# Kernel tuning notes

Measured on AMD Instinct MI355X. Metric: run time of the kernel, lower is better.

Reference implementation:

```python
import jax, jax.numpy as jnp
import numpy as np

B, N, T = 2, 512, 4096
D_MODEL, N_MODES, NODE_H, EDGE_H = 128, 32, 128, 256


def _lin(key, d_in, d_out, scale=0.02):
    kw, kb = jax.random.split(key)
    W = jax.random.normal(kw, (d_in, d_out), jnp.float32) * scale
    b = jax.random.normal(kb, (d_out,), jnp.float32) * scale
    return W, b


def setup_inputs() -> dict:
    key = jax.random.key(0)
    ks = jax.random.split(key, 12)
    spikes = jax.random.normal(ks[0], (B, N, T), jnp.float32)
    # temporal FNO spectral weights (init * 0.01 as in torch)
    Wr = jax.random.normal(ks[1], (N_MODES, D_MODEL), jnp.float32) * 0.01
    Wi = jax.random.normal(ks[2], (N_MODES, D_MODEL), jnp.float32) * 0.01
    pw1, pb1 = _lin(ks[3], D_MODEL, D_MODEL)
    pw2, pb2 = _lin(ks[4], D_MODEL, D_MODEL)
    nw1, nb1 = _lin(ks[5], D_MODEL, NODE_H)
    nw2, nb2 = _lin(ks[6], NODE_H, D_MODEL)
    sw, sb = _lin(ks[7], D_MODEL, EDGE_H)
    tw, tb = _lin(ks[8], D_MODEL, EDGE_H)
    ew1, eb1 = _lin(ks[9], 2 * EDGE_H, EDGE_H)
    ew2, eb2 = _lin(ks[10], EDGE_H, EDGE_H // 2)
    ew3, eb3 = _lin(ks[11], EDGE_H // 2, 2)
    alpha = jnp.asarray(1.0, jnp.float32)
    beta = jnp.asarray(0.0, jnp.float32)
    return dict(spikes=spikes, Wr=Wr, Wi=Wi, pw1=pw1, pb1=pb1, pw2=pw2, pb2=pb2,
                nw1=nw1, nb1=nb1, nw2=nw2, nb2=nb2, sw=sw, sb=sb, tw=tw, tb=tb,
                ew1=ew1, eb1=eb1, ew2=ew2, eb2=eb2, ew3=ew3, eb3=eb3,
                alpha=alpha, beta=beta)


def reference(spikes, Wr, Wi, pw1, pb1, pw2, pb2, nw1, nb1, nw2, nb2,
              sw, sb, tw, tb, ew1, eb1, ew2, eb2, ew3, eb3, alpha, beta):
    relu = jax.nn.relu
    # --- TemporalFourierOperator1D ---
    xf = jnp.fft.rfft(spikes, axis=-1)[..., :N_MODES]          # [B,N,K] complex
    xr, xi = xf.real.astype(spikes.dtype), xf.imag.astype(spikes.dtype)
    # broadcast complex multiply: [B,N,K,1] x [K,D] -> [B,N,K,D]
    yr = xr[..., None] * Wr - xi[..., None] * Wi
    yi = xr[..., None] * Wi + xi[..., None] * Wr
    E = jnp.sqrt(yr * yr + yi * yi + 1e-8).mean(axis=2)         # [B,N,D]
    E = relu(E @ pw1 + pb1) @ pw2 + pb2                          # post_mlp
    # --- NodeFeatureNet ---
    H = relu(relu(E @ nw1 + nb1) @ nw2 + nb2)                    # [B,N,D]
    # --- EdgeFourierCoeffNet ---
    hs = H @ sw + sb                                             # [B,N,Eh]
    ht = H @ tw + tb
    # concat([hs,ht]) @ ew1 == hs @ ew1[:Eh] + ht @ ew1[Eh:] (exact same math)
    ps = hs @ ew1[:EDGE_H]                                       # [B,N,Eh]
    pt = ht @ ew1[EDGE_H:]
    h = relu(ps[:, :, None, :] + pt[:, None, :, :] + eb1)        # [B,N,N,Eh]
    h = relu(h @ ew2 + eb2)                                      # [B,N,N,Eh/2]
    rt = h @ ew3 + eb3                                           # [B,N,N,2]
    coeffs = rt[..., 0] + 1j * rt[..., 1]                        # [B,N,N] complex
    # --- AdjacencyLinearDecoder2D ---
    adj_spatial = jnp.fft.ifft2(coeffs, axes=(-2, -1)).real
    adj_logits = alpha * adj_spatial + beta
    adj_prob = jax.nn.sigmoid(adj_logits)
    return adj_logits, adj_prob
```

## Files before the change

### kernel.cpp

```cpp
#include <hip/hip_runtime.h>
#include <hip/hip_bf16.h>
#include <math.h>

typedef __attribute__((ext_vector_type(8))) short short8;
typedef __attribute__((ext_vector_type(8))) _Float16 f16x8;
typedef __attribute__((ext_vector_type(4))) float f32x4;

__device__ __forceinline__ short f2bf(float x) {
    union { float f; unsigned u; } v; v.f = x;
    unsigned r = v.u + 0x7fffu + ((v.u >> 16) & 1u);
    return (short)(r >> 16);
}
__device__ __forceinline__ unsigned cvtpk(float lo, float hi) {
    unsigned r;
    asm("v_cvt_pk_bf16_f32 %0, %1, %2" : "=v"(r) : "v"(lo), "v"(hi));
    return r;
}
__device__ __forceinline__ unsigned pk_addrelu(unsigned a, unsigned b) {
    unsigned r;
    asm("v_pk_add_f16 %0, %1, %2\n\tv_pk_max_f16 %0, %0, 0"
        : "=v"(r) : "v"(a), "v"(b));
    return r;
}
__device__ __forceinline__ float bflo(unsigned u) {
    union { unsigned u; float f; } v; v.u = u << 16; return v.f;
}
__device__ __forceinline__ float bfhi(unsigned u) {
    union { unsigned u; float f; } v; v.u = u & 0xffff0000u; return v.f;
}
union U32x4 { unsigned u[4]; short8 s8; };
union U32x4H { unsigned u[4]; f16x8 h8; };

__global__ __launch_bounds__(256) void setup_kernel(const float* __restrict__ ew2,
                                                    const float* __restrict__ pw1, const float* __restrict__ pw2,
                                                    const float* __restrict__ nw1, const float* __restrict__ nw2,
                                                    const float* __restrict__ sw, const float* __restrict__ tw,
                                                    const float* __restrict__ sb, const float* __restrict__ tb,
                                                    const float* __restrict__ ew1, const float* __restrict__ eb1,
                                                    short* __restrict__ W4P, short* __restrict__ F1P,
                                                    short* __restrict__ F2, _Float16* __restrict__ EW2H,
                                                    short* __restrict__ PWP,
                                                    short* __restrict__ WCP, float* __restrict__ BC) {
    __shared__ float2 tab[4096];
    __shared__ float eL2[256][32];
    int blk = blockIdx.x, tid = threadIdx.x;
    if (blk < 32) {
        for (int i = tid; i < 4096; i += 256) {
            float sn, cs; sincospif((float)i * (1.0f / 2048.0f), &sn, &cs);
            tab[i] = make_float2(cs, sn);
        }
        __syncthreads();
        int base = blk * 8192;
        #pragma unroll 4
        for (int u = 0; u < 32; ++u) {
            int i = base + u * 256 + tid;
            int j = i & 7, lane = (i >> 3) & 63, nf = (i >> 9) & 3, kkg = i >> 11;
            int k = kkg * 32 + (lane >> 4) * 8 + j;
            int n = nf * 16 + (lane & 15);
            float2 cs = tab[(k * (n & 31)) & 4095];
            W4P[i] = f2bf(n < 32 ? cs.x : -cs.y);
        }
    } else if (blk < 160) {
        for (int i = tid; i < 512; i += 256) {
            float sn, cs; sincospif((float)i * (1.0f / 256.0f), &sn, &cs);
            tab[i] = make_float2(cs, sn);
        }
        __syncthreads();
        int base = (blk - 32) * 8192;
        #pragma unroll 4
        for (int u = 0; u < 32; ++u) {
            int ii = base + u * 256 + tid;
            int j = ii & 7, lane = (ii >> 3) & 63, nfg = (ii >> 9) & 63, kk = ii >> 15;
            int k2 = kk * 32 + (lane >> 4) * 8 + j;
            int t = k2 >> 1, c = k2 & 1;
            int n = nfg * 16 + (lane & 15);
            int q = n >> 1, d = n & 1;
            float2 cs = tab[(t * q) & 511];
            F1P[ii] = f2bf((c == d) ? cs.x : (c ? -cs.y : cs.y));
        }
    } else if (blk < 224) {
        for (int i = tid; i < 512; i += 256) {
            float sn, cs; sincospif((float)i * (1.0f / 256.0f), &sn, &cs);
            tab[i] = make_float2(cs, sn);
        }
        __syncthreads();
        int base = (blk - 160) * 8192;
        #pragma unroll 4
        for (int u = 0; u < 32; ++u) {
            int ii = base + u * 256 + tid;
            int p = ii >> 10, k2 = ii & 1023;
            int s = k2 >> 1, dd = k2 & 1;
            float2 cs = tab[(p * s) & 511];
            F2[ii] = f2bf(dd ? -cs.y : cs.x);
        }
    } else if (blk < 236) {
        int base = (blk - 224) * 8192;
        #pragma unroll 4
        for (int u = 0; u < 32; ++u) {
            int ii = base + u * 256 + tid;
            if (ii < 32768) {
                int j = ii & 7, lane = (ii >> 3) & 63, hf = (ii >> 9) & 7, kk = ii >> 12;
                int k = kk * 32 + (lane >> 4) * 8 + j;
                int h = hf * 16 + (lane & 15);
                EW2H[ii] = (_Float16)ew2[k * 128 + h];
            } else {
                int iw = ii - 32768;
                int l = iw >> 14;
                int r = iw & 16383;
                int j = r & 7, lane = (r >> 3) & 63, nf = (r >> 9) & 7, kk = r >> 12;
                int k = kk * 32 + (lane >> 4) * 8 + j;
                int n = nf * 16 + (lane & 15);
                const float* W = (l == 0) ? pw1 : (l == 1) ? pw2 : (l == 2) ? nw1 : nw2;
                PWP[iw] = f2bf(W[k * 128 + n]);
            }
        }
    } else {
        int blk2 = blk - 236;
        int half = blk2 >> 3, jt = blk2 & 7, j0 = jt * 32;
        const float* ebase = ew1 + (size_t)half * 256 * 256;
        for (int it = 0; it < 32; ++it) {
            int idx = tid + it * 256;
            int i = idx >> 5, jj = idx & 31;
            eL2[i][jj] = ebase[(size_t)i * 256 + j0 + jj];
        }
        __syncthreads();
        const float* wp = half ? tw : sw;
        int d = tid >> 1, jh = tid & 1;
        float acc[16];
        #pragma unroll
        for (int x = 0; x < 16; ++x) acc[x] = 0.f;
        #pragma unroll 4
        for (int i = 0; i < 256; ++i) {
            float wv = wp[(size_t)d * 256 + i];
            #pragma unroll
            for (int x = 0; x < 16; ++x) acc[x] += wv * eL2[i][jh * 16 + x];
        }
        int kk = d >> 5, lg = (d >> 3) & 3, j = d & 7;
        #pragma unroll
        for (int x = 0; x < 16; ++x) {
            int n = half * 256 + j0 + jh * 16 + x;
            int lane = lg * 16 + (n & 15);
            WCP[((kk * 32 + (n >> 4)) * 64 + lane) * 8 + j] = f2bf(acc[x]);
        }
        if (tid < 32) {
            const float* bv = half ? tb : sb;
            float a = 0.f;
            #pragma unroll 8
            for (int i = 0; i < 256; ++i) a += bv[i] * eL2[i][tid];
            if (half == 0) a += eb1[j0 + tid];
            BC[half * 256 + j0 + tid] = a;
        }
    }
}

__global__ __launch_bounds__(256) void dft_mfma(const float* __restrict__ spikes,
                                                const short* __restrict__ W4P,
                                                float* __restrict__ X64P) {
    __shared__ float red[4][4][64][4];
    int part = blockIdx.x & 3;
    int row0 = (blockIdx.x >> 2) * 16;
    int tid = threadIdx.x, wid = tid >> 6, lane = tid & 63;
    int lrow = lane & 15, lg = lane >> 4;

    f32x4 acc[4];
    #pragma unroll
    for (int n = 0; n < 4; ++n) acc[n] = (f32x4){0.f, 0.f, 0.f, 0.f};

    int row = row0 + lrow;
    const float* sbase = spikes + (size_t)row * 4096;
    #pragma unroll
    for (int kk = 0; kk < 8; ++kk) {
        int k = part * 1024 + wid * 256 + kk * 32 + lg * 8;
        const float4* sp = (const float4*)(sbase + k);
        float4 v0 = sp[0], v1 = sp[1];
        U32x4 a;
        a.u[0] = cvtpk(v0.x, v0.y);
        a.u[1] = cvtpk(v0.z, v0.w);
        a.u[2] = cvtpk(v1.x, v1.y);
        a.u[3] = cvtpk(v1.z, v1.w);
        int kkg = part * 32 + wid * 8 + kk;
        #pragma unroll
        for (int n = 0; n < 4; ++n) {
            short8 bfr = *(const short8*)(W4P + ((kkg * 4 + n) * 64 + lane) * 8);
            acc[n] = __builtin_amdgcn_mfma_f32_16x16x32_bf16(a.s8, bfr, acc[n], 0, 0, 0);
        }
    }
    #pragma unroll
    for (int n = 0; n < 4; ++n)
        #pragma unroll
        for (int r = 0; r < 4; ++r) red[wid][n][lane][r] = acc[n][r];
    __syncthreads();
    #pragma unroll
    for (int r = 0; r < 4; ++r) {
        float s = red[0][wid][lane][r] + red[1][wid][lane][r]
                + red[2][wid][lane][r] + red[3][wid][lane][r];
        int orow = row0 + lg * 4 + r;
        X64P[(size_t)part * 65536 + (size_t)orow * 64 + wid * 16 + lrow] = s;
    }
}

__global__ __launch_bounds__(512) void k_node(const float* __restrict__ X64P,
                                              const float* __restrict__ Wr, const float* __restrict__ Wi,
                                              const short* __restrict__ PWP,
                                              const float* __restrict__ pb1, const float* __restrict__ pb2,
                                              const float* __restrict__ nb1, const float* __restrict__ nb2,
                                              const short* __restrict__ WCP, const float* __restrict__ BC,
                                              _Float16* __restrict__ PS16, _Float16* __restrict__ PT16) {
    __shared__ float sx[16][64];
    __shared__ float wri[8192];
    __shared__ short abuf[16 * 128];
    int r0 = blockIdx.x * 16, tid = threadIdx.x;
    int wid = tid >> 6, lane = tid & 63;
    int lrow = lane & 15, lg = lane >> 4;

    #pragma unroll
    for (int it = 0; it < 2; ++it) {
        int idx = tid + it * 512;
        int row = idx >> 6, col = idx & 63;
        float v = 0.f;
        #pragma unroll
        for (int p = 0; p < 4; ++p)
            v += X64P[(size_t)p * 65536 + (size_t)(r0 + row) * 64 + col];
        sx[row][col] = v;
    }
    #pragma unroll
    for (int it = 0; it < 16; ++it) {
        int idx = tid + it * 512;
        wri[idx] = (idx < 4096) ? Wr[idx] : Wi[idx - 4096];
    }
    __syncthreads();

    #pragma unroll
    for (int it = 0; it < 4; ++it) {
        int idx = tid + it * 512;
        int row = idx >> 7, d = idx & 127;
        float acc = 0.f;
        #pragma unroll 8
        for (int k = 0; k < 32; ++k) {
            float a = sx[row][k], b = sx[row][32 + k];
            float wr = wri[k * 128 + d], wi = wri[4096 + k * 128 + d];
            float yr = a * wr - b * wi;
            float yi = a * wi + b * wr;
            acc += sqrtf(yr * yr + yi * yi + 1e-8f);
        }
        abuf[row * 128 + (d ^ ((row & 7) << 3))] = f2bf(acc * (1.0f / 32.0f));
    }
    __syncthreads();

    int asw = (lrow & 7) << 3;
    #pragma unroll 1
    for (int l = 0; l < 4; ++l) {
        f32x4 acc2 = (f32x4){0.f, 0.f, 0.f, 0.f};
        #pragma unroll
        for (int kk = 0; kk < 4; ++kk) {
            short8 a = *(const short8*)(abuf + lrow * 128 + ((kk * 32 + lg * 8) ^ asw));
            short8 b = *(const short8*)(PWP + (((l * 4 + kk) * 8 + wid) * 64 + lane) * 8);
            acc2 = __builtin_amdgcn_mfma_f32_16x16x32_bf16(a, b, acc2, 0, 0, 0);
        }
        __syncthreads();
        const float* bp = (l == 0) ? pb1 : (l == 1) ? pb2 : (l == 2) ? nb1 : nb2;
        bool rl = (l != 1);
        int n = wid * 16 + lrow;
        float bv = bp[n];
        #pragma unroll
        for (int r = 0; r < 4; ++r) {
            int orow = lg * 4 + r;
            float v = acc2[r] + bv;
            if (rl) v = fmaxf(v, 0.f);
            abuf[orow * 128 + (n ^ ((orow & 7) << 3))] = f2bf(v);
        }
        __syncthreads();
    }

    f32x4 acc3[4];
    #pragma unroll
    for (int f = 0; f < 4; ++f) acc3[f] = (f32x4){0.f, 0.f, 0.f, 0.f};
    #pragma unroll
    for (int kk = 0; kk < 4; ++kk) {
        short8 a = *(const short8*)(abuf + lrow * 128 + ((kk * 32 + lg * 8) ^ asw));
        #pragma unroll
        for (int f = 0; f < 4; ++f) {
            short8 b = *(const short8*)(WCP + ((kk * 32 + wid * 4 + f) * 64 + lane) * 8);
            acc3[f] = __builtin_amdgcn_mfma_f32_16x16x32_bf16(a, b, acc3[f], 0, 0, 0);
        }
    }
    #pragma unroll
    for (int f = 0; f < 4; ++f) {
        int n = (wid * 4 + f) * 16 + lrow;
        float bv = BC[n];
        _Float16* dst = (n < 256) ? (PS16 + n) : (PT16 + (n - 256));
        #pragma unroll
        for (int r = 0; r < 4; ++r) {
            int row = r0 + lg * 4 + r;
            dst[(size_t)row * 256] = (_Float16)(acc3[f][r] + bv);
        }
    }
}

__global__ __launch_bounds__(512, 4) void edge_mfma5(
    const unsigned* __restrict__ PS16, const unsigned* __restrict__ PT16,
    const uint4* __restrict__ EW2H4,
    const float* __restrict__ eb2, const float* __restrict__ ew3,
    const float* __restrict__ eb3, unsigned* __restrict__ CCP) {
    __shared__ __align__(16) unsigned ew2s[8192];
    __shared__ __align__(16) unsigned pts[8192];
    __shared__ __align__(16) unsigned pss[2048];
    __shared__ float eb2s[64];
    __shared__ float ew3s[128];

    int bidx = blockIdx.x;
    int ttile = bidx & 7;
    int stile = (bidx >> 3) & 31;
    int b = (bidx >> 8) & 1;
    int hh = bidx >> 9;
    int s0 = stile * 16, t0 = ttile * 64;
    int tid = threadIdx.x;

    { uint4* dst = (uint4*)ew2s;
      #pragma unroll
      for (int it = 0; it < 4; ++it) {
          int idx = tid + it * 512;
          dst[idx] = EW2H4[(idx >> 8) * 512 + hh * 256 + (idx & 255)];
      } }
    { const uint4* src = (const uint4*)(PT16 + (size_t)(b * 512 + t0) * 128);
      uint4* dst = (uint4*)pts;
      #pragma unroll
      for (int it = 0; it < 4; ++it) {
          int idx = tid + it * 512;
          int t = idx >> 5, g = idx & 31;
          dst[t * 32 + (g ^ (t & 7))] = src[idx];
      } }
    { const uint4* src = (const uint4*)(PS16 + (size_t)(b * 512 + s0) * 128);
      ((uint4*)pss)[tid] = src[tid]; }
    if (tid < 64) eb2s[tid] = eb2[hh * 64 + tid];
    if (tid < 128) ew3s[tid] = ew3[hh * 128 + tid];
    __syncthreads();

    int wid = tid >> 6, lane = tid & 63;
    int lrow = lane & 15, lg = lane >> 4;
    float e30 = hh ? 0.f : eb3[0];
    float e31 = hh ? 0.f : eb3[1];
    const uint4* pts4 = (const uint4*)pts;
    const uint4* pss4 = (const uint4*)pss;
    const uint4* ew24 = (const uint4*)ew2s;

    #pragma unroll 1
    for (int i = 0; i < 2; ++i) {
        int s_local = wid * 2 + i;

        f32x4 acc[4][4];
        #pragma unroll
        for (int hf = 0; hf < 4; ++hf)
            #pragma unroll
            for (int tf = 0; tf < 4; ++tf) acc[hf][tf] = (f32x4){0.f, 0.f, 0.f, 0.f};

        #pragma unroll
        for (int kk = 0; kk < 8; ++kk) {
            uint4 pA = pss4[s_local * 32 + kk * 4 + lg];
            f16x8 bf[4];
            #pragma unroll
            for (int tf = 0; tf < 4; ++tf) {
                int t = tf * 16 + lrow;
                uint4 v = pts4[t * 32 + ((kk * 4 + lg) ^ (t & 7))];
                U32x4H r;
                r.u[0] = pk_addrelu(v.x, pA.x);
                r.u[1] = pk_addrelu(v.y, pA.y);
                r.u[2] = pk_addrelu(v.z, pA.z);
                r.u[3] = pk_addrelu(v.w, pA.w);
                bf[tf] = r.h8;
            }
            __builtin_amdgcn_s_setprio(1);
            #pragma unroll
            for (int hf = 0; hf < 4; ++hf) {
                U32x4H af;
                uint4 av = ew24[(kk * 4 + hf) * 64 + lane];
                af.u[0] = av.x; af.u[1] = av.y; af.u[2] = av.z; af.u[3] = av.w;
                #pragma unroll
                for (int tf = 0; tf < 4; ++tf)
                    acc[hf][tf] = __builtin_amdgcn_mfma_f32_16x16x32_f16(af.h8, bf[tf], acc[hf][tf], 0, 0, 0);
            }
            __builtin_amdgcn_s_setprio(0);
        }

        size_t outbase = (size_t)hh * 524288 + (size_t)(b * 512 + s0 + s_local) * 512;
        #pragma unroll
        for (int tf = 0; tf < 4; ++tf) {
            float a0 = 0.f, a1 = 0.f;
            #pragma unroll
            for (int hf = 0; hf < 4; ++hf)
                #pragma unroll
                for (int r = 0; r < 4; ++r) {
                    int hl = hf * 16 + lg * 4 + r;
                    float hv = fmaxf(acc[hf][tf][r] + eb2s[hl], 0.f);
                    a0 += hv * ew3s[2 * hl];
                    a1 += hv * ew3s[2 * hl + 1];
                }
            a0 += __shfl_xor(a0, 16); a1 += __shfl_xor(a1, 16);
            a0 += __shfl_xor(a0, 32); a1 += __shfl_xor(a1, 32);
            if (lg == 0)
                CCP[outbase + t0 + tf * 16 + lrow] = cvtpk(a0 + e30, a1 + e31);
        }
    }
}

__global__ __launch_bounds__(256) void ifft1_mfma(const unsigned* __restrict__ CCP,
                                                  const short* __restrict__ F1P,
                                                  short* __restrict__ B2P) {
    __shared__ short st[32 * 128];
    int bidx = blockIdx.x;
    int nt = bidx & 3;
    int mt = bidx >> 2;
    int bs0 = mt * 16;
    int b = mt >> 5;
    int kk2 = mt & 31;
    int tid = threadIdx.x, wid = tid >> 6, lane = tid & 63;
    int lrow = lane & 15, lg = lane >> 4;

    f32x4 acc[4];
    #pragma unroll
    for (int f = 0; f < 4; ++f) acc[f] = (f32x4){0.f, 0.f, 0.f, 0.f};

    const unsigned* r0p = CCP + (size_t)(bs0 + lrow) * 512 + lg * 4;
    const unsigned* r1p = r0p + 524288;
    #pragma unroll 4
    for (int kk = 0; kk < 32; ++kk) {
        uint4 x0 = *(const uint4*)(r0p + kk * 16);
        uint4 x1 = *(const uint4*)(r1p + kk * 16);
        U32x4 m;
        m.u[0] = cvtpk(bflo(x0.x) + bflo(x1.x), bfhi(x0.x) + bfhi(x1.x));
        m.u[1] = cvtpk(bflo(x0.y) + bflo(x1.y), bfhi(x0.y) + bfhi(x1.y));
        m.u[2] = cvtpk(bflo(x0.z) + bflo(x1.z), bfhi(x0.z) + bfhi(x1.z));
        m.u[3] = cvtpk(bflo(x0.w) + bflo(x1.w), bfhi(x0.w) + bfhi(x1.w));
        #pragma unroll
        for (int f = 0; f < 4; ++f) {
            int nfg = nt * 16 + wid * 4 + f;
            short8 bfr = *(const short8*)(F1P + ((kk * 64 + nfg) * 64 + lane) * 8);
            acc[f] = __builtin_amdgcn_mfma_f32_16x16x32_bf16(m.s8, bfr, acc[f], 0, 0, 0);
        }
    }
    #pragma unroll
    for (int f = 0; f < 4; ++f)
        #pragma unroll
        for (int r = 0; r < 4; ++r) {
            int n_local = (wid * 4 + f) * 16 + lrow;
            int lq = n_local >> 1, d = n_local & 1;
            int lk = (lg * 4 + r) * 2 + d;
            st[lk * 128 + lq] = f2bf(acc[f][r]);
        }
    __syncthreads();
    #pragma unroll
    for (int half = 0; half < 2; ++half) {
        int f2 = (tid >> 6) + half * 4;
        int nf2 = nt * 8 + f2;
        short8 v;
        #pragma unroll
        for (int j = 0; j < 8; ++j)
            v[j] = st[((lane >> 4) * 8 + j) * 128 + f2 * 16 + (lane & 15)];
        *(short8*)(B2P + (size_t)b * 524288 + ((size_t)(kk2 * 32 + nf2) * 64 + lane) * 8) = v;
    }
}

__global__ __launch_bounds__(256) void ifft2_mfma(const short* __restrict__ B2P,
                                                  const short* __restrict__ F2,
                                                  const float* __restrict__ alpha, const float* __restrict__ beta,
                                                  float* __restrict__ out) {
    int bidx = blockIdx.x;
    int pt_ = bidx & 31;
    int qt = (bidx >> 5) & 3;
    int b = bidx >> 7;
    int p0 = pt_ * 16;
    int tid = threadIdx.x, wid = tid >> 6, lane = tid & 63;
    int lrow = lane & 15, lg = lane >> 4;

    f32x4 acc[2];
    acc[0] = (f32x4){0.f, 0.f, 0.f, 0.f};
    acc[1] = (f32x4){0.f, 0.f, 0.f, 0.f};

    const short* arow = F2 + (size_t)(p0 + lrow) * 1024 + lg * 8;
    const short* bbase = B2P + (size_t)b * 524288;
    #pragma unroll 4
    for (int kk = 0; kk < 32; ++kk) {
        short8 a = *(const short8*)(arow + kk * 32);
        #pragma unroll
        for (int f = 0; f < 2; ++f) {
            int nfg = qt * 8 + wid * 2 + f;
            short8 bfr = *(const short8*)(bbase + ((size_t)(kk * 32 + nfg) * 64 + lane) * 8);
            acc[f] = __builtin_amdgcn_mfma_f32_16x16x32_bf16(a, bfr, acc[f], 0, 0, 0);
        }
    }
    float al = alpha[0], be = beta[0];
    const float scale = 1.0f / (512.0f * 512.0f);
    #pragma unroll
    for (int f = 0; f < 2; ++f)
        #pragma unroll
        for (int r = 0; r < 4; ++r) {
            int q = qt * 128 + (wid * 2 + f) * 16 + lrow;
            int p = p0 + lg * 4 + r;
            float l = al * (acc[f][r] * scale) + be;
            size_t idx = (size_t)b * 262144 + (size_t)p * 512 + q;
            out[idx] = l;
            out[524288 + idx] = 1.f / (1.f + expf(-l));
        }
}

extern "C" void kernel_launch(void* const* d_in, const int* in_sizes, int n_in,
                              void* d_out, int out_size, void* d_ws, size_t ws_size,
                              hipStream_t stream) {
    const float* spikes = (const float*)d_in[0];
    const float* Wr  = (const float*)d_in[1];
    const float* Wi  = (const float*)d_in[2];
    const float* pw1 = (const float*)d_in[3];
    const float* pb1 = (const float*)d_in[4];
    const float* pw2 = (const float*)d_in[5];
    const float* pb2 = (const float*)d_in[6];
    const float* nw1 = (const float*)d_in[7];
    const float* nb1 = (const float*)d_in[8];
    const float* nw2 = (const float*)d_in[9];
    const float* nb2 = (const float*)d_in[10];
    const float* sw  = (const float*)d_in[11];
    const float* sb  = (const float*)d_in[12];
    const float* tw_ = (const float*)d_in[13];
    const float* tb  = (const float*)d_in[14];
    const float* ew1 = (const float*)d_in[15];
    const float* eb1 = (const float*)d_in[16];
    const float* ew2 = (const float*)d_in[17];
    const float* eb2 = (const float*)d_in[18];
    const float* ew3 = (const float*)d_in[19];
    const float* eb3 = (const float*)d_in[20];
    const float* alpha = (const float*)d_in[21];
    const float* beta  = (const float*)d_in[22];
    float* out = (float*)d_out;
    float* ws  = (float*)d_ws;

    unsigned* CCP = (unsigned*)d_out;

    float*    X64P = ws + 0;
    short*    WCP  = (short*)(ws + 262144);
    float*    BC   = ws + 294912;
    _Float16* PS16 = (_Float16*)(ws + 295424);
    _Float16* PT16 = (_Float16*)(ws + 426496);
    short*    B2P  = (short*)(ws + 0);
    _Float16* EW2H = (_Float16*)(ws + 557568);
    short*    W4P  = (short*)(ws + 573952);
    short*    F1P  = (short*)(ws + 705024);
    short*    F2   = (short*)(ws + 1229312);
    short*    PWP  = (short*)(ws + 1491456);

    setup_kernel<<<252, 256, 0, stream>>>(ew2, pw1, pw2, nw1, nw2, sw, tw_, sb, tb, ew1, eb1,
                                          W4P, F1P, F2, EW2H, PWP, WCP, BC);
    dft_mfma<<<256, 256, 0, stream>>>(spikes, W4P, X64P);
    k_node<<<64, 512, 0, stream>>>(X64P, Wr, Wi, PWP, pb1, pb2, nb1, nb2, WCP, BC, PS16, PT16);
    edge_mfma5<<<1024, 512, 0, stream>>>((const unsigned*)PS16, (const unsigned*)PT16,
                                         (const uint4*)EW2H, eb2, ew3, eb3, CCP);
    ifft1_mfma<<<256, 256, 0, stream>>>(CCP, F1P, B2P);
    ifft2_mfma<<<256, 256, 0, stream>>>(B2P, F2, alpha, beta, out);
}
```

Before: 128.1 us.

## Double grid sizes of DFT and IFFT kernels; stream edge weights from global memory

```diff
diff --git a/kernel.cpp b/kernel.cpp
--- a/kernel.cpp
+++ b/kernel.cpp
@@ -157,8 +157,8 @@
                                                 const short* __restrict__ W4P,
                                                 float* __restrict__ X64P) {
     __shared__ float red[4][4][64][4];
-    int part = blockIdx.x & 3;
-    int row0 = (blockIdx.x >> 2) * 16;
+    int part = blockIdx.x & 7;
+    int row0 = (blockIdx.x >> 3) * 16;
     int tid = threadIdx.x, wid = tid >> 6, lane = tid & 63;
     int lrow = lane & 15, lg = lane >> 4;
 
@@ -169,8 +169,8 @@
     int row = row0 + lrow;
     const float* sbase = spikes + (size_t)row * 4096;
     #pragma unroll
-    for (int kk = 0; kk < 8; ++kk) {
-        int k = part * 1024 + wid * 256 + kk * 32 + lg * 8;
+    for (int kk = 0; kk < 4; ++kk) {
+        int k = part * 512 + wid * 128 + kk * 32 + lg * 8;
         const float4* sp = (const float4*)(sbase + k);
         float4 v0 = sp[0], v1 = sp[1];
         U32x4 a;
@@ -178,7 +178,7 @@
         a.u[1] = cvtpk(v0.z, v0.w);
         a.u[2] = cvtpk(v1.x, v1.y);
         a.u[3] = cvtpk(v1.z, v1.w);
-        int kkg = part * 32 + wid * 8 + kk;
+        int kkg = part * 16 + wid * 4 + kk;
         #pragma unroll
         for (int n = 0; n < 4; ++n) {
             short8 bfr = *(const short8*)(W4P + ((kkg * 4 + n) * 64 + lane) * 8);
@@ -219,7 +219,7 @@
         int row = idx >> 6, col = idx & 63;
         float v = 0.f;
         #pragma unroll
-        for (int p = 0; p < 4; ++p)
+        for (int p = 0; p < 8; ++p)
             v += X64P[(size_t)p * 65536 + (size_t)(r0 + row) * 64 + col];
         sx[row][col] = v;
     }
@@ -297,12 +297,11 @@
     }
 }
 
-__global__ __launch_bounds__(512, 4) void edge_mfma5(
+__global__ __launch_bounds__(512, 4) void edge_mfma6(
     const unsigned* __restrict__ PS16, const unsigned* __restrict__ PT16,
     const uint4* __restrict__ EW2H4,
     const float* __restrict__ eb2, const float* __restrict__ ew3,
     const float* __restrict__ eb3, unsigned* __restrict__ CCP) {
-    __shared__ __align__(16) unsigned ew2s[8192];
     __shared__ __align__(16) unsigned pts[8192];
     __shared__ __align__(16) unsigned pss[2048];
     __shared__ float eb2s[64];
@@ -316,12 +315,6 @@
     int s0 = stile * 16, t0 = ttile * 64;
     int tid = threadIdx.x;
 
-    { uint4* dst = (uint4*)ew2s;
-      #pragma unroll
-      for (int it = 0; it < 4; ++it) {
-          int idx = tid + it * 512;
-          dst[idx] = EW2H4[(idx >> 8) * 512 + hh * 256 + (idx & 255)];
-      } }
     { const uint4* src = (const uint4*)(PT16 + (size_t)(b * 512 + t0) * 128);
       uint4* dst = (uint4*)pts;
       #pragma unroll
@@ -342,7 +335,7 @@
     float e31 = hh ? 0.f : eb3[1];
     const uint4* pts4 = (const uint4*)pts;
     const uint4* pss4 = (const uint4*)pss;
-    const uint4* ew24 = (const uint4*)ew2s;
+    const uint4* ew2g = EW2H4 + hh * 256 + lane;
 
     #pragma unroll 1
     for (int i = 0; i < 2; ++i) {
@@ -357,6 +350,10 @@
         #pragma unroll
         for (int kk = 0; kk < 8; ++kk) {
             uint4 pA = pss4[s_local * 32 + kk * 4 + lg];
+            uint4 av0 = ew2g[kk * 512];
+            uint4 av1 = ew2g[kk * 512 + 64];
+            uint4 av2 = ew2g[kk * 512 + 128];
+            uint4 av3 = ew2g[kk * 512 + 192];
             f16x8 bf[4];
             #pragma unroll
             for (int tf = 0; tf < 4; ++tf) {
@@ -373,7 +370,7 @@
             #pragma unroll
             for (int hf = 0; hf < 4; ++hf) {
                 U32x4H af;
-                uint4 av = ew24[(kk * 4 + hf) * 64 + lane];
+                uint4 av = (hf == 0) ? av0 : (hf == 1) ? av1 : (hf == 2) ? av2 : av3;
                 af.u[0] = av.x; af.u[1] = av.y; af.u[2] = av.z; af.u[3] = av.w;
                 #pragma unroll
                 for (int tf = 0; tf < 4; ++tf)
@@ -406,19 +403,19 @@
 __global__ __launch_bounds__(256) void ifft1_mfma(const unsigned* __restrict__ CCP,
                                                   const short* __restrict__ F1P,
                                                   short* __restrict__ B2P) {
-    __shared__ short st[32 * 128];
+    __shared__ short st[32 * 64];
     int bidx = blockIdx.x;
-    int nt = bidx & 3;
-    int mt = bidx >> 2;
+    int nt = bidx & 7;
+    int mt = bidx >> 3;
     int bs0 = mt * 16;
     int b = mt >> 5;
     int kk2 = mt & 31;
     int tid = threadIdx.x, wid = tid >> 6, lane = tid & 63;
     int lrow = lane & 15, lg = lane >> 4;
 
-    f32x4 acc[4];
-    #pragma unroll
-    for (int f = 0; f < 4; ++f) acc[f] = (f32x4){0.f, 0.f, 0.f, 0.f};
+    f32x4 acc[2];
+    acc[0] = (f32x4){0.f, 0.f, 0.f, 0.f};
+    acc[1] = (f32x4){0.f, 0.f, 0.f, 0.f};
 
     const unsigned* r0p = CCP + (size_t)(bs0 + lrow) * 512 + lg * 4;
     const unsigned* r1p = r0p + 524288;
@@ -432,30 +429,29 @@
         m.u[2] = cvtpk(bflo(x0.z) + bflo(x1.z), bfhi(x0.z) + bfhi(x1.z));
         m.u[3] = cvtpk(bflo(x0.w) + bflo(x1.w), bfhi(x0.w) + bfhi(x1.w));
         #pragma unroll
-        for (int f = 0; f < 4; ++f) {
-            int nfg = nt * 16 + wid * 4 + f;
+        for (int f = 0; f < 2; ++f) {
+            int nfg = nt * 8 + wid * 2 + f;
             short8 bfr = *(const short8*)(F1P + ((kk * 64 + nfg) * 64 + lane) * 8);
             acc[f] = __builtin_amdgcn_mfma_f32_16x16x32_bf16(m.s8, bfr, acc[f], 0, 0, 0);
         }
     }
     #pragma unroll
-    for (int f = 0; f < 4; ++f)
+    for (int f = 0; f < 2; ++f)
         #pragma unroll
         for (int r = 0; r < 4; ++r) {
-            int n_local = (wid * 4 + f) * 16 + lrow;
+            int n_local = (wid * 2 + f) * 16 + lrow;
             int lq = n_local >> 1, d = n_local & 1;
             int lk = (lg * 4 + r) * 2 + d;
-            st[lk * 128 + lq] = f2bf(acc[f][r]);
+            st[lk * 64 + lq] = f2bf(acc[f][r]);
         }
     __syncthreads();
-    #pragma unroll
-    for (int half = 0; half < 2; ++half) {
-        int f2 = (tid >> 6) + half * 4;
-        int nf2 = nt * 8 + f2;
+    {
+        int f2 = wid;
+        int nf2 = nt * 4 + f2;
         short8 v;
         #pragma unroll
         for (int j = 0; j < 8; ++j)
-            v[j] = st[((lane >> 4) * 8 + j) * 128 + f2 * 16 + (lane & 15)];
+            v[j] = st[((lane >> 4) * 8 + j) * 64 + f2 * 16 + (lane & 15)];
         *(short8*)(B2P + (size_t)b * 524288 + ((size_t)(kk2 * 32 + nf2) * 64 + lane) * 8) = v;
     }
 }
@@ -466,41 +462,34 @@
                                                   float* __restrict__ out) {
     int bidx = blockIdx.x;
     int pt_ = bidx & 31;
-    int qt = (bidx >> 5) & 3;
-    int b = bidx >> 7;
+    int qt = (bidx >> 5) & 7;
+    int b = bidx >> 8;
     int p0 = pt_ * 16;
     int tid = threadIdx.x, wid = tid >> 6, lane = tid & 63;
     int lrow = lane & 15, lg = lane >> 4;
 
-    f32x4 acc[2];
-    acc[0] = (f32x4){0.f, 0.f, 0.f, 0.f};
-    acc[1] = (f32x4){0.f, 0.f, 0.f, 0.f};
+    f32x4 acc = (f32x4){0.f, 0.f, 0.f, 0.f};
 
     const short* arow = F2 + (size_t)(p0 + lrow) * 1024 + lg * 8;
     const short* bbase = B2P + (size_t)b * 524288;
+    int nfg = qt * 4 + wid;
     #pragma unroll 4
     for (int kk = 0; kk < 32; ++kk) {
         short8 a = *(const short8*)(arow + kk * 32);
-        #pragma unroll
-        for (int f = 0; f < 2; ++f) {
-            int nfg = qt * 8 + wid * 2 + f;
-            short8 bfr = *(const short8*)(bbase + ((size_t)(kk * 32 + nfg) * 64 + lane) * 8);
-            acc[f] = __builtin_amdgcn_mfma_f32_16x16x32_bf16(a, bfr, acc[f], 0, 0, 0);
-        }
+        short8 bfr = *(const short8*)(bbase + ((size_t)(kk * 32 + nfg) * 64 + lane) * 8);
+        acc = __builtin_amdgcn_mfma_f32_16x16x32_bf16(a, bfr, acc, 0, 0, 0);
     }
     float al = alpha[0], be = beta[0];
     const float scale = 1.0f / (512.0f * 512.0f);
     #pragma unroll
-    for (int f = 0; f < 2; ++f)
-        #pragma unroll
-        for (int r = 0; r < 4; ++r) {
-            int q = qt * 128 + (wid * 2 + f) * 16 + lrow;
-            int p = p0 + lg * 4 + r;
-            float l = al * (acc[f][r] * scale) + be;
-            size_t idx = (size_t)b * 262144 + (size_t)p * 512 + q;
-            out[idx] = l;
-            out[524288 + idx] = 1.f / (1.f + expf(-l));
-        }
+    for (int r = 0; r < 4; ++r) {
+        int q = qt * 64 + wid * 16 + lrow;
+        int p = p0 + lg * 4 + r;
+        float l = al * (acc[r] * scale) + be;
+        size_t idx = (size_t)b * 262144 + (size_t)p * 512 + q;
+        out[idx] = l;
+        out[524288 + idx] = 1.f / (1.f + expf(-l));
+    }
 }
 
 extern "C" void kernel_launch(void* const* d_in, const int* in_sizes, int n_in,
@@ -532,26 +521,25 @@
     float* out = (float*)d_out;
     float* ws  = (float*)d_ws;
 
-    unsigned* CCP = (unsigned*)d_out;
-
-    float*    X64P = ws + 0;
-    short*    WCP  = (short*)(ws + 262144);
-    float*    BC   = ws + 294912;
-    _Float16* PS16 = (_Float16*)(ws + 295424);
-    _Float16* PT16 = (_Float16*)(ws + 426496);
-    short*    B2P  = (short*)(ws + 0);
-    _Float16* EW2H = (_Float16*)(ws + 557568);
-    short*    W4P  = (short*)(ws + 573952);
-    short*    F1P  = (short*)(ws + 705024);
-    short*    F2   = (short*)(ws + 1229312);
-    short*    PWP  = (short*)(ws + 1491456);
+    unsigned* CCP   = (unsigned*)(ws + 0);
+    float*    X64P  = ws + 0;
+    short*    WCP   = (short*)(ws + 524288);
+    float*    BC    = ws + 557056;
+    _Float16* PS16  = (_Float16*)(ws + 1048576);
+    _Float16* PT16  = (_Float16*)(ws + 1179648);
+    short*    B2P   = (short*)(ws + 1048576);
+    _Float16* EW2H  = (_Float16*)(ws + 1572864);
+    short*    W4P   = (short*)(ws + 1589248);
+    short*    F1P   = (short*)(ws + 1720320);
+    short*    F2    = (short*)(ws + 2244608);
+    short*    PWP   = (short*)(ws + 2506752);
 
     setup_kernel<<<252, 256, 0, stream>>>(ew2, pw1, pw2, nw1, nw2, sw, tw_, sb, tb, ew1, eb1,
                                           W4P, F1P, F2, EW2H, PWP, WCP, BC);
-    dft_mfma<<<256, 256, 0, stream>>>(spikes, W4P, X64P);
+    dft_mfma<<<512, 256, 0, stream>>>(spikes, W4P, X64P);
     k_node<<<64, 512, 0, stream>>>(X64P, Wr, Wi, PWP, pb1, pb2, nb1, nb2, WCP, BC, PS16, PT16);
-    edge_mfma5<<<1024, 512, 0, stream>>>((const unsigned*)PS16, (const unsigned*)PT16,
+    edge_mfma6<<<1024, 512, 0, stream>>>((const unsigned*)PS16, (const unsigned*)PT16,
                                          (const uint4*)EW2H, eb2, ew3, eb3, CCP);
-    ifft1_mfma<<<256, 256, 0, stream>>>(CCP, F1P, B2P);
-    ifft2_mfma<<<256, 256, 0, stream>>>(B2P, F2, alpha, beta, out);
-}
+    ifft1_mfma<<<512, 256, 0, stream>>>(CCP, F1P, B2P);
+    ifft2_mfma<<<512, 256, 0, stream>>>(B2P, F2, alpha, beta, out);
+}
```

New measurement: 185.5 us. +44.8%, slower.
